# Kernel tuning notes

Measured on AMD Instinct MI355X. Metric: run time of the kernel, lower is better.

## Reference

```python
import jax, jax.numpy as jnp
import numpy as np

B, N, M = 4, 4096, 4096  # samples, pred pts/sample, target pts/sample
LOSS_WEIGHT = 1.0


def setup_inputs() -> dict:
    key = jax.random.key(0)
    k1, k2, k3 = jax.random.split(key, 3)
    pred_pc = jax.random.normal(k1, (B * N, 3), dtype=jnp.float32)
    target = jax.random.normal(k2, (B * M, 3), dtype=jnp.float32)
    label = jax.random.randint(k3, (B * N,), 0, 2)  # binary keep-mask per pred point
    nums = jnp.full((B,), N, dtype=jnp.int32)        # uniform ragged sizes (static for jit)
    dense_nums = jnp.full((B,), M, dtype=jnp.int32)
    return {"pred_pc": pred_pc, "target": target, "label": label,
            "nums": nums, "dense_nums": dense_nums}


def reference(pred_pc, target, label, nums, dense_nums):
    b = nums.shape[0]
    p = pred_pc.reshape(b, -1, 3)      # [B,N,3]
    t = target.reshape(b, -1, 3)       # [B,M,3]
    mask = (label.reshape(b, -1) == 1) # [B,N] valid pred points

    # squared pairwise distances via |p|^2 + |t|^2 - 2 p.t  -> [B,N,M]
    pn = jnp.sum(p * p, axis=-1)
    tn = jnp.sum(t * t, axis=-1)
    d = pn[:, :, None] + tn[:, None, :] - 2.0 * jnp.einsum('bnd,bmd->bnm', p, t)
    d = jnp.maximum(d, 0.0)

    # pred -> target: min over M, L1 (sqrt before mean), masked mean over valid preds
    d1 = jnp.sqrt(jnp.min(d, axis=2))                              # [B,N]
    cnt = jnp.maximum(jnp.sum(mask, axis=1), 1)
    m1 = jnp.sum(jnp.where(mask, d1, 0.0), axis=1) / cnt           # [B]

    # target -> pred: min over valid pred points only (invalid rows masked to +big)
    BIG = jnp.float32(1e10)
    d2 = jnp.sqrt(jnp.min(jnp.where(mask[:, :, None], d, BIG), axis=1))  # [B,M]
    m2 = jnp.mean(d2, axis=1)                                      # [B]

    per_sample = 0.5 * (m1 + m2)   # ChamferDistanceL1: (d1.mean()+d2.mean())/2
    return jnp.mean(per_sample) * LOSS_WEIGHT
```

## Files before the change

kernel.cpp:

```cpp
#include <hip/hip_runtime.h>

#define TPB   256
#define QPT   4
#define SPLIT 16

#define POISON 1.0e5f

__global__ void __launch_bounds__(TPB) init_mins(unsigned int* w, int n1, int n2) {
    int i = blockIdx.x * blockDim.x + threadIdx.x;
    if (i < n1) {
        w[i] = __float_as_uint(3.0e38f);
    } else if (i < n1 + n2) {
        w[i] = __float_as_uint(1.0e10f);
    }
}

__global__ void __launch_bounds__(TPB) nn_fused(
    const float* __restrict__ pred,
    const float* __restrict__ target,
    const int*   __restrict__ label,
    unsigned int* __restrict__ min1,
    unsigned int* __restrict__ min2,
    int N, int M, int natmax)
{
    __shared__ float4 tile[TPB];

    const int dir = blockIdx.z;
    const float* __restrict__ A  = dir ? target : pred;
    const float* __restrict__ Bp = dir ? pred   : target;
    const int NA = dir ? M : N;
    const int NB = dir ? N : M;
    const int* __restrict__ labB = dir ? label : nullptr;
    unsigned int* __restrict__ outm = dir ? min2 : min1;

    const int natiles = (NA + TPB * QPT - 1) / (TPB * QPT);
    const int b  = blockIdx.x / natmax;
    const int at = blockIdx.x - b * natmax;
    if (at >= natiles) return;

    const size_t abase = (size_t)b * NA;

    float px[QPT], py[QPT], pz[QPT], best[QPT];
#pragma unroll
    for (int q = 0; q < QPT; ++q) {
        int a = at * (TPB * QPT) + q * TPB + threadIdx.x;
        int idx = (a < NA) ? a : 0;
        const float* sp = A + (abase + idx) * 3;
        px[q] = sp[0];
        py[q] = sp[1];
        pz[q] = sp[2];
        best[q] = 3.0e38f;
    }

    const int slen = (NB + SPLIT - 1) / SPLIT;
    const int sbeg = blockIdx.y * slen;
    const int send = min(sbeg + slen, NB);
    const size_t bbase = (size_t)b * NB;

    for (int c = sbeg; c < send; c += TPB) {
        int m = c + threadIdx.x;
        float4 qv = make_float4(POISON, 0.0f, 0.0f, 0.0f);
        if (m < send) {
            const float* sp = Bp + (bbase + m) * 3;
            float x = sp[0], y = sp[1], z = sp[2];
            if (labB != nullptr && labB[bbase + m] != 1) x = POISON;
            qv = make_float4(x, y, z, 0.0f);
        }
        __syncthreads();
        tile[threadIdx.x] = qv;
        __syncthreads();

        const int jn = min(send - c, TPB);
        if (jn == TPB) {
#pragma unroll 16
            for (int j = 0; j < TPB; ++j) {
                float4 t = tile[j];
#pragma unroll
                for (int q = 0; q < QPT; ++q) {
                    float dx = px[q] - t.x;
                    float dy = py[q] - t.y;
                    float dz = pz[q] - t.z;
                    float d = fmaf(dx, dx, fmaf(dy, dy, dz * dz));
                    best[q] = fminf(best[q], d);
                }
            }
        } else {
            for (int j = 0; j < jn; ++j) {
                float4 t = tile[j];
#pragma unroll
                for (int q = 0; q < QPT; ++q) {
                    float dx = px[q] - t.x;
                    float dy = py[q] - t.y;
                    float dz = pz[q] - t.z;
                    float d = fmaf(dx, dx, fmaf(dy, dy, dz * dz));
                    best[q] = fminf(best[q], d);
                }
            }
        }
    }

#pragma unroll
    for (int q = 0; q < QPT; ++q) {
        int a = at * (TPB * QPT) + q * TPB + threadIdx.x;
        if (a < NA) {
            atomicMin(&outm[abase + a], __float_as_uint(best[q]));
        }
    }
}

__device__ float block_reduce_sum(float v, float* red) {
    int tid = threadIdx.x;
    red[tid] = v;
    __syncthreads();
    for (int s = TPB / 2; s > 0; s >>= 1) {
        if (tid < s) red[tid] += red[tid + s];
        __syncthreads();
    }
    float r = red[0];
    __syncthreads();
    return r;
}

__global__ void __launch_bounds__(TPB) partial_kernel(
    const unsigned int* __restrict__ min1,
    const unsigned int* __restrict__ min2,
    const int* __restrict__ label,
    float* __restrict__ s1, float* __restrict__ c1, float* __restrict__ s2,
    int B, int N, int M, int ptN, int ptM)
{
    __shared__ float red[TPB];
    const int r = blockIdx.x;
    const int regionN = B * ptN;

    if (r < regionN) {
        int b = r / ptN;
        int t = r - b * ptN;
        int n = t * TPB + threadIdx.x;
        float s = 0.0f, cc = 0.0f;
        if (n < N) {
            size_t i = (size_t)b * N + n;
            if (label[i] == 1) {
                s = sqrtf(__uint_as_float(min1[i]));
                cc = 1.0f;
            }
        }
        s  = block_reduce_sum(s, red);
        cc = block_reduce_sum(cc, red);
        if (threadIdx.x == 0) { s1[r] = s; c1[r] = cc; }
    } else {
        int r2 = r - regionN;
        int b = r2 / ptM;
        int t = r2 - b * ptM;
        int m = t * TPB + threadIdx.x;
        float s = 0.0f;
        if (m < M) {
            s = sqrtf(__uint_as_float(min2[(size_t)b * M + m]));
        }
        s = block_reduce_sum(s, red);
        if (threadIdx.x == 0) s2[r2] = s;
    }
}

__global__ void __launch_bounds__(64) final_kernel(
    const float* __restrict__ s1, const float* __restrict__ c1,
    const float* __restrict__ s2,
    float* __restrict__ out, int B, int M, int ptN, int ptM)
{
    __shared__ float acc[64];
    int tid = threadIdx.x;
    float v = 0.0f;
    if (tid < B) {
        float S1 = 0.0f, C1 = 0.0f, S2 = 0.0f;
        for (int i = 0; i < ptN; ++i) { S1 += s1[tid * ptN + i]; C1 += c1[tid * ptN + i]; }
        for (int i = 0; i < ptM; ++i) { S2 += s2[tid * ptM + i]; }
        float m1 = S1 / fmaxf(C1, 1.0f);
        float m2 = S2 / (float)M;
        v = 0.5f * (m1 + m2);
    }
    acc[tid] = v;
    __syncthreads();
    if (tid == 0) {
        float a = 0.0f;
        for (int b = 0; b < B; ++b) a += acc[b];
        out[0] = a / (float)B;
    }
}

extern "C" void kernel_launch(void* const* d_in, const int* in_sizes, int n_in,
                              void* d_out, int out_size, void* d_ws, size_t ws_size,
                              hipStream_t stream) {
    const float* pred   = (const float*)d_in[0];
    const float* target = (const float*)d_in[1];
    const int*   label  = (const int*)  d_in[2];

    const int B = in_sizes[3];
    const int N = in_sizes[2] / B;
    const int M = in_sizes[1] / (3 * B);

    unsigned int* min1 = (unsigned int*)d_ws;
    unsigned int* min2 = min1 + (size_t)B * N;
    const int ptN = (N + TPB - 1) / TPB;
    const int ptM = (M + TPB - 1) / TPB;
    float* s1 = (float*)(min2 + (size_t)B * M);
    float* c1 = s1 + (size_t)B * ptN;
    float* s2 = c1 + (size_t)B * ptN;

    const int total = B * (N + M);
    init_mins<<<(total + TPB - 1) / TPB, TPB, 0, stream>>>(min1, B * N, B * M);

    const int nat1 = (N + TPB * QPT - 1) / (TPB * QPT);
    const int nat2 = (M + TPB * QPT - 1) / (TPB * QPT);
    const int natmax = max(nat1, nat2);
    dim3 g(B * natmax, SPLIT, 2);
    nn_fused<<<g, TPB, 0, stream>>>(pred, target, label, min1, min2, N, M, natmax);

    const int nred = B * (ptN + ptM);
    partial_kernel<<<nred, TPB, 0, stream>>>(min1, min2, label, s1, c1, s2,
                                             B, N, M, ptN, ptM);

    final_kernel<<<1, 64, 0, stream>>>(s1, c1, s2, (float*)d_out, B, M, ptN, ptM);
}
```

Before: 37.40 us.

## Use norm-expansion distance, per-split min buffers instead of atomics, retile

Rewrites the inner distance as |t|^2 - 2 p·t, with target norms precomputed in the tile's w slot, so each pair costs three FMAs and a min instead of subtracts plus FMAs. Masked points get a huge norm in place of a poisoned coordinate. Atomic mins and the init kernel are replaced by per-split partial-min buffers that the reduction kernel min-reduces across 32 splits. Tiling changes to 128 threads x 8 queries with 32 splits, which means more workspace traffic and a possible loss of precision from the expanded form.

```diff
diff --git a/kernel.cpp b/kernel.cpp
--- a/kernel.cpp
+++ b/kernel.cpp
@@ -1,27 +1,16 @@
 #include <hip/hip_runtime.h>
 
-#define TPB   256
-#define QPT   4
-#define SPLIT 16
-
-#define POISON 1.0e5f
-
-__global__ void __launch_bounds__(TPB) init_mins(unsigned int* w, int n1, int n2) {
-    int i = blockIdx.x * blockDim.x + threadIdx.x;
-    if (i < n1) {
-        w[i] = __float_as_uint(3.0e38f);
-    } else if (i < n1 + n2) {
-        w[i] = __float_as_uint(1.0e10f);
-    }
-}
-
-__global__ void __launch_bounds__(TPB) nn_fused(
+#define TPB   128
+#define QPT   8
+#define SPLIT 32
+#define RTPB  256
+
+__global__ void __launch_bounds__(TPB) nn_kernel(
     const float* __restrict__ pred,
     const float* __restrict__ target,
     const int*   __restrict__ label,
-    unsigned int* __restrict__ min1,
-    unsigned int* __restrict__ min2,
-    int N, int M, int natmax)
+    float* __restrict__ minsplit,
+    int B, int N, int M, int natmax, int stride)
 {
     __shared__ float4 tile[TPB];
 
@@ -31,7 +20,6 @@
     const int NA = dir ? M : N;
     const int NB = dir ? N : M;
     const int* __restrict__ labB = dir ? label : nullptr;
-    unsigned int* __restrict__ outm = dir ? min2 : min1;
 
     const int natiles = (NA + TPB * QPT - 1) / (TPB * QPT);
     const int b  = blockIdx.x / natmax;
@@ -40,7 +28,7 @@
 
     const size_t abase = (size_t)b * NA;
 
-    float px[QPT], py[QPT], pz[QPT], best[QPT];
+    float px[QPT], py[QPT], pz[QPT], pn[QPT], best[QPT];
 #pragma unroll
     for (int q = 0; q < QPT; ++q) {
         int a = at * (TPB * QPT) + q * TPB + threadIdx.x;
@@ -49,6 +37,7 @@
         px[q] = sp[0];
         py[q] = sp[1];
         pz[q] = sp[2];
+        pn[q] = fmaf(px[q], px[q], fmaf(py[q], py[q], pz[q] * pz[q]));
         best[q] = 3.0e38f;
     }
 
@@ -59,51 +48,51 @@
 
     for (int c = sbeg; c < send; c += TPB) {
         int m = c + threadIdx.x;
-        float4 qv = make_float4(POISON, 0.0f, 0.0f, 0.0f);
+        float4 qv = make_float4(0.0f, 0.0f, 0.0f, 1.0e10f);
         if (m < send) {
             const float* sp = Bp + (bbase + m) * 3;
             float x = sp[0], y = sp[1], z = sp[2];
-            if (labB != nullptr && labB[bbase + m] != 1) x = POISON;
-            qv = make_float4(x, y, z, 0.0f);
+            float tn = fmaf(x, x, fmaf(y, y, z * z));
+            if (labB != nullptr && labB[bbase + m] != 1) {
+                x = 0.0f; y = 0.0f; z = 0.0f; tn = 1.0e10f;
+            }
+            qv = make_float4(x, y, z, tn);
         }
         __syncthreads();
         tile[threadIdx.x] = qv;
         __syncthreads();
 
         const int jn = min(send - c, TPB);
-        if (jn == TPB) {
-#pragma unroll 16
-            for (int j = 0; j < TPB; ++j) {
-                float4 t = tile[j];
-#pragma unroll
-                for (int q = 0; q < QPT; ++q) {
-                    float dx = px[q] - t.x;
-                    float dy = py[q] - t.y;
-                    float dz = pz[q] - t.z;
-                    float d = fmaf(dx, dx, fmaf(dy, dy, dz * dz));
-                    best[q] = fminf(best[q], d);
-                }
-            }
-        } else {
-            for (int j = 0; j < jn; ++j) {
-                float4 t = tile[j];
-#pragma unroll
-                for (int q = 0; q < QPT; ++q) {
-                    float dx = px[q] - t.x;
-                    float dy = py[q] - t.y;
-                    float dz = pz[q] - t.z;
-                    float d = fmaf(dx, dx, fmaf(dy, dy, dz * dz));
-                    best[q] = fminf(best[q], d);
-                }
-            }
-        }
-    }
-
+        const int jeven = jn & ~1;
+#pragma unroll 8
+        for (int j = 0; j < jeven; j += 2) {
+            float4 t0 = tile[j];
+            float4 t1 = tile[j + 1];
+#pragma unroll
+            for (int q = 0; q < QPT; ++q) {
+                float s0 = fmaf(px[q], t0.x, fmaf(py[q], t0.y, pz[q] * t0.z));
+                float s1 = fmaf(px[q], t1.x, fmaf(py[q], t1.y, pz[q] * t1.z));
+                float v0 = fmaf(-2.0f, s0, t0.w);
+                float v1 = fmaf(-2.0f, s1, t1.w);
+                best[q] = fminf(best[q], fminf(v0, v1));
+            }
+        }
+        if (jn & 1) {
+            float4 t0 = tile[jn - 1];
+#pragma unroll
+            for (int q = 0; q < QPT; ++q) {
+                float s0 = fmaf(px[q], t0.x, fmaf(py[q], t0.y, pz[q] * t0.z));
+                best[q] = fminf(best[q], fmaf(-2.0f, s0, t0.w));
+            }
+        }
+    }
+
+    float* out = minsplit + (((size_t)dir * B + b) * SPLIT + blockIdx.y) * stride;
 #pragma unroll
     for (int q = 0; q < QPT; ++q) {
         int a = at * (TPB * QPT) + q * TPB + threadIdx.x;
         if (a < NA) {
-            atomicMin(&outm[abase + a], __float_as_uint(best[q]));
+            out[a] = fmaxf(best[q] + pn[q], 0.0f);
         }
     }
 }
@@ -112,7 +101,7 @@
     int tid = threadIdx.x;
     red[tid] = v;
     __syncthreads();
-    for (int s = TPB / 2; s > 0; s >>= 1) {
+    for (int s = RTPB / 2; s > 0; s >>= 1) {
         if (tid < s) red[tid] += red[tid + s];
         __syncthreads();
     }
@@ -121,26 +110,29 @@
     return r;
 }
 
-__global__ void __launch_bounds__(TPB) partial_kernel(
-    const unsigned int* __restrict__ min1,
-    const unsigned int* __restrict__ min2,
+__global__ void __launch_bounds__(RTPB) partial_kernel(
+    const float* __restrict__ minsplit,
     const int* __restrict__ label,
     float* __restrict__ s1, float* __restrict__ c1, float* __restrict__ s2,
-    int B, int N, int M, int ptN, int ptM)
+    int B, int N, int M, int ptN, int ptM, int stride)
 {
-    __shared__ float red[TPB];
+    __shared__ float red[RTPB];
     const int r = blockIdx.x;
     const int regionN = B * ptN;
 
     if (r < regionN) {
         int b = r / ptN;
         int t = r - b * ptN;
-        int n = t * TPB + threadIdx.x;
+        int n = t * RTPB + threadIdx.x;
         float s = 0.0f, cc = 0.0f;
         if (n < N) {
-            size_t i = (size_t)b * N + n;
-            if (label[i] == 1) {
-                s = sqrtf(__uint_as_float(min1[i]));
+            const float* base = minsplit + ((size_t)b * SPLIT) * stride + n;
+            float m = base[0];
+            for (int sp = 1; sp < SPLIT; ++sp) {
+                m = fminf(m, base[(size_t)sp * stride]);
+            }
+            if (label[(size_t)b * N + n] == 1) {
+                s = sqrtf(m);
                 cc = 1.0f;
             }
         }
@@ -151,10 +143,15 @@
         int r2 = r - regionN;
         int b = r2 / ptM;
         int t = r2 - b * ptM;
-        int m = t * TPB + threadIdx.x;
+        int mq = t * RTPB + threadIdx.x;
         float s = 0.0f;
-        if (m < M) {
-            s = sqrtf(__uint_as_float(min2[(size_t)b * M + m]));
+        if (mq < M) {
+            const float* base = minsplit + (((size_t)B + b) * SPLIT) * stride + mq;
+            float m = base[0];
+            for (int sp = 1; sp < SPLIT; ++sp) {
+                m = fminf(m, base[(size_t)sp * stride]);
+            }
+            s = sqrtf(m);
         }
         s = block_reduce_sum(s, red);
         if (threadIdx.x == 0) s2[r2] = s;
@@ -197,26 +194,25 @@
     const int N = in_sizes[2] / B;
     const int M = in_sizes[1] / (3 * B);
 
-    unsigned int* min1 = (unsigned int*)d_ws;
-    unsigned int* min2 = min1 + (size_t)B * N;
-    const int ptN = (N + TPB - 1) / TPB;
-    const int ptM = (M + TPB - 1) / TPB;
-    float* s1 = (float*)(min2 + (size_t)B * M);
+    const int stride = (N > M) ? N : M;
+
+    float* minsplit = (float*)d_ws;
+    const int ptN = (N + RTPB - 1) / RTPB;
+    const int ptM = (M + RTPB - 1) / RTPB;
+    float* s1 = minsplit + (size_t)2 * B * SPLIT * stride;
     float* c1 = s1 + (size_t)B * ptN;
     float* s2 = c1 + (size_t)B * ptN;
 
-    const int total = B * (N + M);
-    init_mins<<<(total + TPB - 1) / TPB, TPB, 0, stream>>>(min1, B * N, B * M);
-
     const int nat1 = (N + TPB * QPT - 1) / (TPB * QPT);
     const int nat2 = (M + TPB * QPT - 1) / (TPB * QPT);
-    const int natmax = max(nat1, nat2);
+    const int natmax = (nat1 > nat2) ? nat1 : nat2;
     dim3 g(B * natmax, SPLIT, 2);
-    nn_fused<<<g, TPB, 0, stream>>>(pred, target, label, min1, min2, N, M, natmax);
+    nn_kernel<<<g, TPB, 0, stream>>>(pred, target, label, minsplit,
+                                     B, N, M, natmax, stride);
 
     const int nred = B * (ptN + ptM);
-    partial_kernel<<<nred, TPB, 0, stream>>>(min1, min2, label, s1, c1, s2,
-                                             B, N, M, ptN, ptM);
+    partial_kernel<<<nred, RTPB, 0, stream>>>(minsplit, label, s1, c1, s2,
+                                              B, N, M, ptN, ptM, stride);
 
     final_kernel<<<1, 64, 0, stream>>>(s1, c1, s2, (float*)d_out, B, M, ptN, ptM);
 }
```

After: 35.58 us. 4.9% less time.
